# Performance work log

Hardware: AMD Instinct MI355X
Metric: run time of the kernel (lower is better)

Reference implementation:

```python
import jax, jax.numpy as jnp
import numpy as np

B, N, H, NH = 8, 1024, 512, 8
HD = H // NH
SCALE = float(np.sqrt(HD))


def setup_inputs() -> dict:
    key = jax.random.key(0)
    ks = jax.random.split(key, 14)
    s = 0.02
    return {
        "x": jax.random.normal(ks[0], (B, N, H), jnp.float32),
        "distance_matrix": jax.random.uniform(ks[1], (B, N, N), jnp.float32),
        "mask": jax.random.randint(ks[2], (B, N), 0, 2).astype(bool),
        "Wq": jax.random.normal(ks[3], (H, H), jnp.float32) * s,
        "bq": jnp.zeros((H,), jnp.float32),
        "Wk": jax.random.normal(ks[4], (H, H), jnp.float32) * s,
        "bk": jnp.zeros((H,), jnp.float32),
        "Wv": jax.random.normal(ks[5], (H, H), jnp.float32) * s,
        "bv": jnp.zeros((H,), jnp.float32),
        "Wo": jax.random.normal(ks[6], (H, H), jnp.float32) * s,
        "bo": jnp.zeros((H,), jnp.float32),
        "dist_emb": jax.random.normal(ks[7], (50, NH), jnp.float32) * s,
        "attn_bias": jnp.zeros((NH, 1, 1), jnp.float32),
    }


def reference(x, distance_matrix, mask, Wq, bq, Wk, bk, Wv, bv, Wo, bo, dist_emb, attn_bias):
    Bb, Nn, _ = x.shape
    # projections (torch Linear: x @ W.T + b), split heads -> [B, N, NH, HD]
    Q = (x @ Wq.T + bq).reshape(Bb, Nn, NH, HD)
    K = (x @ Wk.T + bk).reshape(Bb, Nn, NH, HD)
    V = (x @ Wv.T + bv).reshape(Bb, Nn, NH, HD)
    # scores [B, NH, N, N]
    scores = jnp.einsum('bqhd,bkhd->bhqk', Q, K) / SCALE
    # distance-bin bias lookup: [B,N,N] -> bins -> [B,N,N,NH] -> [B,NH,N,N]
    bins = jnp.clip((distance_matrix * 10.0).astype(jnp.int32), 0, 49)
    dbias = jnp.transpose(dist_emb[bins], (0, 3, 1, 2))
    scores = scores + dbias + attn_bias[None]  # attn_bias [NH,1,1] broadcasts
    scores = jnp.where(mask[:, None, None, :], -1e9, scores)  # mask over keys
    attn = jax.nn.softmax(scores, axis=-1)  # dropout = identity in eval
    out = jnp.einsum('bhqk,bkhd->bqhd', attn, V).reshape(Bb, Nn, H)
    return out @ Wo.T + bo
```

## Files before the change

kernel.cpp:

```cpp
#include <hip/hip_runtime.h>
#include <hip/hip_bf16.h>
#include <math.h>

#define B_  8
#define N_  1024
#define H_  512
#define NH_ 8
#define HD_ 64

typedef __attribute__((ext_vector_type(8))) short short8;
typedef __attribute__((ext_vector_type(4))) short short4_t;
typedef __attribute__((ext_vector_type(4))) float floatx4;

#define GPTR(p) ((const __attribute__((address_space(1))) void*)(p))
#define LPTR(p) ((__attribute__((address_space(3))) void*)(p))

#define TRB16(dst, addr, IMM) \
    asm volatile("ds_read_b64_tr_b16 %0, %1 offset:" IMM \
                 : "=v"(dst) : "v"(addr) : "memory")

#define EXP2(x) exp2f(x)
#define LOG2E 1.44269504088896f

static __device__ __forceinline__ unsigned short f2bf(float f) {
    __hip_bfloat16 h = __float2bfloat16(f);
    unsigned short u;
    __builtin_memcpy(&u, &h, 2);
    return u;
}

__global__ __launch_bounds__(256) void cvt_all(
    const float* __restrict__ x,  const float* __restrict__ wq,
    const float* __restrict__ wk, const float* __restrict__ wv,
    const float* __restrict__ wo, unsigned short* __restrict__ dst)
{
    const int n4 = (4194304 + 4 * 262144) / 4;
    int i = blockIdx.x * blockDim.x + threadIdx.x;
    const int stride = gridDim.x * blockDim.x;
    for (; i < n4; i += stride) {
        const int e = i * 4;
        const float* src;
        if (e < 4194304) {
            src = x + e;
        } else {
            const int rel = e - 4194304;
            const int w = rel >> 18;
            const int off = rel & 262143;
            src = (w == 0 ? wq : w == 1 ? wk : w == 2 ? wv : wo) + off;
        }
        const float4 v = *(const float4*)src;
        ushort4 r;
        r.x = f2bf(v.x); r.y = f2bf(v.y); r.z = f2bf(v.z); r.w = f2bf(v.w);
        *(ushort4*)(dst + e) = r;
    }
}

__global__ __launch_bounds__(256) void bins_kernel(
    const float* __restrict__ dist, const int* __restrict__ mask,
    unsigned char* __restrict__ bins)
{
    const int gid = blockIdx.x * 256 + threadIdx.x;
    const size_t e = (size_t)gid * 16;
    const int b = gid >> 16;
    const int k = (gid & 63) * 16;
    const float* dsrc = dist + e;
    const int*   msrc = mask + b * N_ + k;

    unsigned w[4];
    #pragma unroll
    for (int i = 0; i < 4; ++i) {
        const float4 v = *(const float4*)(dsrc + 4 * i);
        const int4  mm = *(const int4*)(msrc + 4 * i);
        int b0 = (int)(v.x * 10.f); b0 = b0 < 0 ? 0 : (b0 > 49 ? 49 : b0);
        int b1 = (int)(v.y * 10.f); b1 = b1 < 0 ? 0 : (b1 > 49 ? 49 : b1);
        int b2 = (int)(v.z * 10.f); b2 = b2 < 0 ? 0 : (b2 > 49 ? 49 : b2);
        int b3 = (int)(v.w * 10.f); b3 = b3 < 0 ? 0 : (b3 > 49 ? 49 : b3);
        if (mm.x) b0 = 255;
        if (mm.y) b1 = 255;
        if (mm.z) b2 = 255;
        if (mm.w) b3 = 255;
        w[i] = (unsigned)b0 | ((unsigned)b1 << 8) | ((unsigned)b2 << 16) | ((unsigned)b3 << 24);
    }
    uint4 u; u.x = w[0]; u.y = w[1]; u.z = w[2]; u.w = w[3];
    *(uint4*)(bins + e) = u;
}

template <int BF16OUT>
static __device__ __forceinline__ void gemm_core(
    const unsigned short* __restrict__ A, const unsigned short* __restrict__ W,
    const float* __restrict__ bias, void* __restrict__ C,
    int Ncols, int K, float scale, int row0, int col0)
{
    __shared__ unsigned short As[128 * 32];
    __shared__ unsigned short Bs[128 * 32];

    const int t    = threadIdx.x;
    const int lane = t & 63;
    const int wave = t >> 6;
    const int wr   = wave >> 1;
    const int wc   = wave & 1;
    const int l15  = lane & 15;
    const int lhi  = lane >> 4;

    const int srow = wave * 32 + (lane >> 2);
    const int sk   = (lane & 3) * 8;
    const unsigned short* gA = A + (size_t)(row0 + srow) * K + sk;
    const unsigned short* gB = W + (size_t)(col0 + srow) * K + sk;

    floatx4 acc[4][4];
    #pragma unroll
    for (int m = 0; m < 4; ++m)
        #pragma unroll
        for (int n = 0; n < 4; ++n) acc[m][n] = (floatx4)0.f;

    for (int k0 = 0; k0 < K; k0 += 32) {
        __syncthreads();
        #pragma unroll
        for (int i = 0; i < 2; ++i) {
            __builtin_amdgcn_global_load_lds(GPTR(gA + (size_t)(i * 16) * K + k0),
                                             LPTR(&As[(wave * 32 + i * 16) * 32]), 16, 0, 0);
            __builtin_amdgcn_global_load_lds(GPTR(gB + (size_t)(i * 16) * K + k0),
                                             LPTR(&Bs[(wave * 32 + i * 16) * 32]), 16, 0, 0);
        }
        __syncthreads();

        short8 af[4], bf[4];
        #pragma unroll
        for (int m = 0; m < 4; ++m)
            af[m] = *(const short8*)&As[(wr * 64 + m * 16 + l15) * 32 + lhi * 8];
        #pragma unroll
        for (int n = 0; n < 4; ++n)
            bf[n] = *(const short8*)&Bs[(wc * 64 + n * 16 + l15) * 32 + lhi * 8];
        #pragma unroll
        for (int m = 0; m < 4; ++m)
            #pragma unroll
            for (int n = 0; n < 4; ++n)
                acc[m][n] = __builtin_amdgcn_mfma_f32_16x16x32_bf16(af[m], bf[n], acc[m][n], 0, 0, 0);
    }

    #pragma unroll
    for (int n = 0; n < 4; ++n) {
        const int col = col0 + wc * 64 + n * 16 + l15;
        const float bvv = bias[col];
        #pragma unroll
        for (int m = 0; m < 4; ++m) {
            #pragma unroll
            for (int r = 0; r < 4; ++r) {
                const int row = row0 + wr * 64 + m * 16 + lhi * 4 + r;
                const float v = (acc[m][n][r] + bvv) * scale;
                if (BF16OUT)
                    ((unsigned short*)C)[(size_t)row * Ncols + col] = f2bf(v);
                else
                    ((float*)C)[(size_t)row * Ncols + col] = v;
            }
        }
    }
}

__global__ __launch_bounds__(256) void gemm_qkv(
    const unsigned short* __restrict__ xb,
    const unsigned short* __restrict__ Wq, const unsigned short* __restrict__ Wk,
    const unsigned short* __restrict__ Wv,
    const float* __restrict__ bq, const float* __restrict__ bk,
    const float* __restrict__ bv,
    unsigned short* __restrict__ Qb, unsigned short* __restrict__ Kb,
    unsigned short* __restrict__ Vb)
{
    const int z = blockIdx.z;
    const unsigned short* W = z == 0 ? Wq : (z == 1 ? Wk : Wv);
    const float* bias       = z == 0 ? bq : (z == 1 ? bk : bv);
    unsigned short* C       = z == 0 ? Qb : (z == 1 ? Kb : Vb);
    const float scale       = z == 0 ? (0.125f * LOG2E) : 1.0f;
    gemm_core<1>(xb, W, bias, C, H_, H_, scale, blockIdx.y * 128, blockIdx.x * 128);
}

__global__ __launch_bounds__(256) void gemm_out(
    const unsigned short* __restrict__ Ab, const unsigned short* __restrict__ Wo,
    const float* __restrict__ bo, float* __restrict__ out)
{
    gemm_core<0>(Ab, Wo, bo, out, H_, H_, 1.0f, blockIdx.y * 128, blockIdx.x * 128);
}

__global__ __launch_bounds__(256) void attn_mfma(
    const unsigned short* __restrict__ Qg, const unsigned short* __restrict__ Kg,
    const unsigned short* __restrict__ Vg, const unsigned char* __restrict__ bins,
    const float* __restrict__ demb, const float* __restrict__ abias,
    unsigned short* __restrict__ O)
{
    const int qt = blockIdx.x;
    const int h  = blockIdx.y;
    const int b  = blockIdx.z;
    const int q0 = qt * 64;
    const int t  = threadIdx.x;
    const int lane = t & 63;
    const int wave = t >> 6;
    const int l15 = lane & 15;
    const int lhi = lane >> 4;

    __shared__ unsigned short Ks[64 * 64];
    __shared__ unsigned short Vs[64 * 64];
    __shared__ unsigned short QPs[64 * 64];
    __shared__ unsigned char  Bs[64 * 80];

    float dbl = -1.442695e9f;
    if (lane < 50) dbl = (demb[lane * NH_ + h] + abias[h]) * LOG2E;

    const unsigned short* ksrc[2];
    const unsigned short* vsrc[2];
    #pragma unroll
    for (int i = 0; i < 2; ++i) {
        const int C = wave * 128 + i * 64 + lane;
        const int kr = C >> 3, c = C & 7;
        ksrc[i] = Kg + ((size_t)(b * N_) + kr) * H_ + h * HD_ + ((c ^ (kr & 7)) * 8);
        const int vd16 = C >> 7, rem = C & 127;
        const int krhi = rem >> 3, r2 = rem & 7;
        const int vkr = krhi * 4 + (r2 >> 1), vc = r2 & 1;
        vsrc[i] = Vg + ((size_t)(b * N_) + vkr) * H_ + h * HD_ + vd16 * 16 + vc * 8;
    }
    const unsigned char* bsrc = bins + ((size_t)(b * N_) + q0 + (t >> 2)) * N_ + (t & 3) * 16;
    const int bidx = (t >> 2) * 80 + (t & 3) * 16;

    {
        const int qr = t >> 2;
        const int d0 = (t & 3) * 16;
        const unsigned short* src = Qg + ((size_t)(b * N_ + q0 + qr)) * H_ + h * HD_ + d0;
        #pragma unroll
        for (int cc = 0; cc < 2; ++cc) {
            const uint4 v = *(const uint4*)(src + 8 * cc);
            const int idx = (qr * 64 + d0 + 8 * cc) ^ ((qr & 7) << 3);
            *(uint4*)&QPs[idx] = v;
        }
    }
    __syncthreads();

    short8 aq[2];
    {
        const int qrow = (wave << 4) + l15;
        #pragma unroll
        for (int ck = 0; ck < 2; ++ck) {
            const int kb = lhi * 8 + 32 * ck;
            const int idx = (qrow * 64 + kb) ^ ((qrow & 7) << 3);
            aq[ck] = *(const short8*)&QPs[idx];
        }
    }
    __syncthreads();

    unsigned short* const Pw = &QPs[wave << 10];
    const unsigned trlane = (unsigned)(lhi << 8) + (unsigned)(l15 << 3);
    const unsigned vaddr = (unsigned)(size_t)LPTR(&Vs[0]) + trlane;

    float m = -INFINITY, lsum = 0.f;
    floatx4 o4[4];
    #pragma unroll
    for (int nd = 0; nd < 4; ++nd) o4[nd] = (floatx4)0.f;

    for (int k0 = 0; k0 < N_; k0 += 64) {
        __syncthreads();
        {
            const size_t koff = (size_t)k0;
            #pragma unroll
            for (int i = 0; i < 2; ++i) {
                __builtin_amdgcn_global_load_lds(GPTR(ksrc[i] + koff * H_),
                    LPTR(&Ks[(wave * 128 + i * 64) * 8]), 16, 0, 0);
                __builtin_amdgcn_global_load_lds(GPTR(vsrc[i] + koff * H_),
                    LPTR(&Vs[(wave * 128 + i * 64) * 8]), 16, 0, 0);
            }
            const uint4 brv = *(const uint4*)(bsrc + koff);
            *(uint4*)&Bs[bidx] = brv;
        }
        __syncthreads();

        floatx4 s4[4];
        __builtin_amdgcn_s_setprio(1);
        #pragma unroll
        for (int kn = 0; kn < 4; ++kn) {
            const int kcol = kn * 16 + l15;
            floatx4 acc = (floatx4)0.f;
            #pragma unroll
            for (int ck = 0; ck < 2; ++ck) {
                const int kb = lhi * 8 + 32 * ck;
                const int idx = (kcol * 64 + kb) ^ ((kcol & 7) << 3);
                const short8 bk = *(const short8*)&Ks[idx];
                acc = __builtin_amdgcn_mfma_f32_16x16x32_bf16(bk, aq[ck], acc, 0, 0, 0);
            }
            s4[kn] = acc;
        }
        __builtin_amdgcn_s_setprio(0);

        #pragma unroll
        for (int kn = 0; kn < 4; ++kn) {
            const unsigned bb =
                *(const unsigned*)&Bs[((wave << 4) + l15) * 80 + kn * 16 + (lhi << 2)];
            s4[kn][0] += __shfl(dbl, (int)(bb & 255u), 64);
            s4[kn][1] += __shfl(dbl, (int)((bb >> 8) & 255u), 64);
            s4[kn][2] += __shfl(dbl, (int)((bb >> 16) & 255u), 64);
            s4[kn][3] += __shfl(dbl, (int)(bb >> 24), 64);
        }

        {
            float mx = s4[0][0];
            #pragma unroll
            for (int kn = 0; kn < 4; ++kn)
                #pragma unroll
                for (int r = 0; r < 4; ++r) mx = fmaxf(mx, s4[kn][r]);
            mx = fmaxf(mx, __shfl_xor(mx, 16, 64));
            mx = fmaxf(mx, __shfl_xor(mx, 32, 64));
            const float mnew = fmaxf(m, mx);
            float ts = 0.f;
            #pragma unroll
            for (int kn = 0; kn < 4; ++kn)
                #pragma unroll
                for (int r = 0; r < 4; ++r) {
                    const float p = EXP2(s4[kn][r] - mnew);
                    s4[kn][r] = p;
                    ts += p;
                }
            ts += __shfl_xor(ts, 16, 64);
            ts += __shfl_xor(ts, 32, 64);
            const float alpha = EXP2(m - mnew);
            lsum = lsum * alpha + ts;
            m = mnew;
            #pragma unroll
            for (int r = 0; r < 4; ++r) {
                const float ar = __shfl(alpha, lhi * 4 + r, 64);
                #pragma unroll
                for (int nd = 0; nd < 4; ++nd) o4[nd][r] *= ar;
            }
        }

        #pragma unroll
        for (int kn = 0; kn < 4; ++kn) {
            short4_t pk;
            pk[0] = (short)f2bf(s4[kn][0]);
            pk[1] = (short)f2bf(s4[kn][1]);
            pk[2] = (short)f2bf(s4[kn][2]);
            pk[3] = (short)f2bf(s4[kn][3]);
            const int idx = (l15 * 64 + kn * 16 + (lhi << 2)) ^ ((l15 & 7) << 3);
            *(short4_t*)&Pw[idx] = pk;
        }

        short8 ap[2];
        #pragma unroll
        for (int ck = 0; ck < 2; ++ck) {
            const int idx = (l15 * 64 + ck * 32 + lhi * 8) ^ ((l15 & 7) << 3);
            ap[ck] = *(const short8*)&Pw[idx];
        }
        short4_t v0l[4], v0h[4], v1l[4], v1h[4];
        TRB16(v0l[0], vaddr, "0");    TRB16(v0h[0], vaddr, "128");
        TRB16(v0l[1], vaddr, "2048"); TRB16(v0h[1], vaddr, "2176");
        TRB16(v0l[2], vaddr, "4096"); TRB16(v0h[2], vaddr, "4224");
        TRB16(v0l[3], vaddr, "6144"); TRB16(v0h[3], vaddr, "6272");
        TRB16(v1l[0], vaddr, "1024"); TRB16(v1h[0], vaddr, "1152");
        TRB16(v1l[1], vaddr, "3072"); TRB16(v1h[1], vaddr, "3200");
        TRB16(v1l[2], vaddr, "5120"); TRB16(v1h[2], vaddr, "5248");
        TRB16(v1l[3], vaddr, "7168"); TRB16(v1h[3], vaddr, "7296");
        asm volatile("s_waitcnt lgkmcnt(0)" ::: "memory");
        __builtin_amdgcn_sched_barrier(0);

        __builtin_amdgcn_s_setprio(1);
        #pragma unroll
        for (int nd = 0; nd < 4; ++nd) {
            const short8 bv0 = __builtin_shufflevector(v0l[nd], v0h[nd], 0, 1, 2, 3, 4, 5, 6, 7);
            o4[nd] = __builtin_amdgcn_mfma_f32_16x16x32_bf16(ap[0], bv0, o4[nd], 0, 0, 0);
            const short8 bv1 = __builtin_shufflevector(v1l[nd], v1h[nd], 0, 1, 2, 3, 4, 5, 6, 7);
            o4[nd] = __builtin_amdgcn_mfma_f32_16x16x32_bf16(ap[1], bv1, o4[nd], 0, 0, 0);
        }
        __builtin_amdgcn_s_setprio(0);
    }

    float inv[4];
    #pragma unroll
    for (int r = 0; r < 4; ++r) inv[r] = 1.f / __shfl(lsum, lhi * 4 + r, 64);
    #pragma unroll
    for (int nd = 0; nd < 4; ++nd) {
        const int d = nd * 16 + l15;
        #pragma unroll
        for (int r = 0; r < 4; ++r) {
            const int q = q0 + (wave << 4) + lhi * 4 + r;
            O[((size_t)(b * N_ + q)) * H_ + h * HD_ + d] = f2bf(o4[nd][r] * inv[r]);
        }
    }
}

extern "C" void kernel_launch(void* const* d_in, const int* in_sizes, int n_in,
                              void* d_out, int out_size, void* d_ws, size_t ws_size,
                              hipStream_t stream)
{
    const float* x    = (const float*)d_in[0];
    const float* dist = (const float*)d_in[1];
    const int*   mask = (const int*)d_in[2];
    const float* Wq   = (const float*)d_in[3];
    const float* bq   = (const float*)d_in[4];
    const float* Wk   = (const float*)d_in[5];
    const float* bk   = (const float*)d_in[6];
    const float* Wv   = (const float*)d_in[7];
    const float* bv   = (const float*)d_in[8];
    const float* Wo   = (const float*)d_in[9];
    const float* bo   = (const float*)d_in[10];
    const float* demb = (const float*)d_in[11];
    const float* ab   = (const float*)d_in[12];
    float* out = (float*)d_out;

    const size_t mat = (size_t)B_ * N_ * H_;
    const size_t wsz = (size_t)H_ * H_;

    unsigned short* blob = (unsigned short*)d_ws;
    unsigned short* xb  = blob;
    unsigned short* Wqb = blob + mat;
    unsigned short* Wkb = Wqb + wsz;
    unsigned short* Wvb = Wkb + wsz;
    unsigned short* Wob = Wvb + wsz;
    unsigned short* Qb  = Wob + wsz;
    unsigned short* Kb  = Qb + mat;
    unsigned short* Vb  = Kb + mat;
    unsigned short* Ab  = Vb + mat;
    unsigned char*  binsb = (unsigned char*)(Ab + mat);

    const dim3 blk(256);

    hipLaunchKernelGGL(cvt_all, dim3(1024), blk, 0, stream, x, Wq, Wk, Wv, Wo, blob);
    hipLaunchKernelGGL(bins_kernel, dim3((B_ * N_ * N_) / 16 / 256), blk, 0, stream,
                       dist, mask, binsb);

    const dim3 qgrid(H_ / 128, (B_ * N_) / 128, 3);
    hipLaunchKernelGGL(gemm_qkv, qgrid, blk, 0, stream,
                       xb, Wqb, Wkb, Wvb, bq, bk, bv, Qb, Kb, Vb);

    const dim3 agrid(N_ / 64, NH_, B_);
    hipLaunchKernelGGL(attn_mfma, agrid, blk, 0, stream,
                       Qb, Kb, Vb, binsb, demb, ab, Ab);

    const dim3 ogrid(H_ / 128, (B_ * N_) / 128, 1);
    hipLaunchKernelGGL(gemm_out, ogrid, blk, 0, stream, Ab, Wob, bo, out);
}
```

Measured before the change: 109.5 us.

## Fuse prep kernels, register-prefetch distance bins, skip softmax rescale when max is stable

Merges the bf16 conversion and bin-computation kernels into one launch, partitioned by block index. In the attention kernel, bins are read straight from global memory into registers and prefetched one tile ahead, removing the LDS staging buffer. The online softmax now skips the output rescale when no row max has grown by more than 8 (log2 units) past the running max. This keeps the old max, so probabilities can exceed 1 before normalisation, which adds a small overflow or precision risk.

```diff
diff --git a/kernel.cpp b/kernel.cpp
--- a/kernel.cpp
+++ b/kernel.cpp
@@ -29,60 +29,58 @@
     return u;
 }
 
-__global__ __launch_bounds__(256) void cvt_all(
+__global__ __launch_bounds__(256) void prep_kernel(
     const float* __restrict__ x,  const float* __restrict__ wq,
     const float* __restrict__ wk, const float* __restrict__ wv,
-    const float* __restrict__ wo, unsigned short* __restrict__ dst)
-{
-    const int n4 = (4194304 + 4 * 262144) / 4;
-    int i = blockIdx.x * blockDim.x + threadIdx.x;
-    const int stride = gridDim.x * blockDim.x;
-    for (; i < n4; i += stride) {
-        const int e = i * 4;
-        const float* src;
-        if (e < 4194304) {
-            src = x + e;
-        } else {
-            const int rel = e - 4194304;
-            const int w = rel >> 18;
-            const int off = rel & 262143;
-            src = (w == 0 ? wq : w == 1 ? wk : w == 2 ? wv : wo) + off;
-        }
-        const float4 v = *(const float4*)src;
-        ushort4 r;
-        r.x = f2bf(v.x); r.y = f2bf(v.y); r.z = f2bf(v.z); r.w = f2bf(v.w);
-        *(ushort4*)(dst + e) = r;
-    }
-}
-
-__global__ __launch_bounds__(256) void bins_kernel(
+    const float* __restrict__ wo, unsigned short* __restrict__ dst,
     const float* __restrict__ dist, const int* __restrict__ mask,
     unsigned char* __restrict__ bins)
 {
-    const int gid = blockIdx.x * 256 + threadIdx.x;
-    const size_t e = (size_t)gid * 16;
-    const int b = gid >> 16;
-    const int k = (gid & 63) * 16;
-    const float* dsrc = dist + e;
-    const int*   msrc = mask + b * N_ + k;
-
-    unsigned w[4];
-    #pragma unroll
-    for (int i = 0; i < 4; ++i) {
-        const float4 v = *(const float4*)(dsrc + 4 * i);
-        const int4  mm = *(const int4*)(msrc + 4 * i);
-        int b0 = (int)(v.x * 10.f); b0 = b0 < 0 ? 0 : (b0 > 49 ? 49 : b0);
-        int b1 = (int)(v.y * 10.f); b1 = b1 < 0 ? 0 : (b1 > 49 ? 49 : b1);
-        int b2 = (int)(v.z * 10.f); b2 = b2 < 0 ? 0 : (b2 > 49 ? 49 : b2);
-        int b3 = (int)(v.w * 10.f); b3 = b3 < 0 ? 0 : (b3 > 49 ? 49 : b3);
-        if (mm.x) b0 = 255;
-        if (mm.y) b1 = 255;
-        if (mm.z) b2 = 255;
-        if (mm.w) b3 = 255;
-        w[i] = (unsigned)b0 | ((unsigned)b1 << 8) | ((unsigned)b2 << 16) | ((unsigned)b3 << 24);
-    }
-    uint4 u; u.x = w[0]; u.y = w[1]; u.z = w[2]; u.w = w[3];
-    *(uint4*)(bins + e) = u;
+    const int bid = blockIdx.x;
+    if (bid < 1280) {
+        const int n4 = (4194304 + 4 * 262144) / 4;
+        int i = bid * 256 + threadIdx.x;
+        for (; i < n4; i += 1280 * 256) {
+            const int e = i * 4;
+            const float* src;
+            if (e < 4194304) {
+                src = x + e;
+            } else {
+                const int rel = e - 4194304;
+                const int w = rel >> 18;
+                const int off = rel & 262143;
+                src = (w == 0 ? wq : w == 1 ? wk : w == 2 ? wv : wo) + off;
+            }
+            const float4 v = *(const float4*)src;
+            ushort4 r;
+            r.x = f2bf(v.x); r.y = f2bf(v.y); r.z = f2bf(v.z); r.w = f2bf(v.w);
+            *(ushort4*)(dst + e) = r;
+        }
+    } else {
+        const int gid = (bid - 1280) * 256 + threadIdx.x;
+        const size_t e = (size_t)gid * 16;
+        const int b = gid >> 16;
+        const int k = (gid & 63) * 16;
+        const float* dsrc = dist + e;
+        const int*   msrc = mask + b * N_ + k;
+        unsigned w[4];
+        #pragma unroll
+        for (int i = 0; i < 4; ++i) {
+            const float4 v = *(const float4*)(dsrc + 4 * i);
+            const int4  mm = *(const int4*)(msrc + 4 * i);
+            int b0 = (int)(v.x * 10.f); b0 = b0 < 0 ? 0 : (b0 > 49 ? 49 : b0);
+            int b1 = (int)(v.y * 10.f); b1 = b1 < 0 ? 0 : (b1 > 49 ? 49 : b1);
+            int b2 = (int)(v.z * 10.f); b2 = b2 < 0 ? 0 : (b2 > 49 ? 49 : b2);
+            int b3 = (int)(v.w * 10.f); b3 = b3 < 0 ? 0 : (b3 > 49 ? 49 : b3);
+            if (mm.x) b0 = 255;
+            if (mm.y) b1 = 255;
+            if (mm.z) b2 = 255;
+            if (mm.w) b3 = 255;
+            w[i] = (unsigned)b0 | ((unsigned)b1 << 8) | ((unsigned)b2 << 16) | ((unsigned)b3 << 24);
+        }
+        uint4 u; u.x = w[0]; u.y = w[1]; u.z = w[2]; u.w = w[3];
+        *(uint4*)(bins + e) = u;
+    }
 }
 
 template <int BF16OUT>
@@ -200,7 +198,6 @@
     __shared__ unsigned short Ks[64 * 64];
     __shared__ unsigned short Vs[64 * 64];
     __shared__ unsigned short QPs[64 * 64];
-    __shared__ unsigned char  Bs[64 * 80];
 
     float dbl = -1.442695e9f;
     if (lane < 50) dbl = (demb[lane * NH_ + h] + abias[h]) * LOG2E;
@@ -217,8 +214,8 @@
         const int vkr = krhi * 4 + (r2 >> 1), vc = r2 & 1;
         vsrc[i] = Vg + ((size_t)(b * N_) + vkr) * H_ + h * HD_ + vd16 * 16 + vc * 8;
     }
-    const unsigned char* bsrc = bins + ((size_t)(b * N_) + q0 + (t >> 2)) * N_ + (t & 3) * 16;
-    const int bidx = (t >> 2) * 80 + (t & 3) * 16;
+    const unsigned char* bbase =
+        bins + ((size_t)(b * N_) + q0 + (wave << 4) + l15) * N_ + (lhi << 2);
 
     {
         const int qr = t >> 2;
@@ -231,6 +228,10 @@
             *(uint4*)&QPs[idx] = v;
         }
     }
+    unsigned brC[4], brN[4];
+    #pragma unroll
+    for (int kn = 0; kn < 4; ++kn)
+        brC[kn] = *(const unsigned*)(bbase + kn * 16);
     __syncthreads();
 
     short8 aq[2];
@@ -254,7 +255,8 @@
     #pragma unroll
     for (int nd = 0; nd < 4; ++nd) o4[nd] = (floatx4)0.f;
 
-    for (int k0 = 0; k0 < N_; k0 += 64) {
+    for (int tt = 0; tt < 16; ++tt) {
+        const int k0 = tt * 64;
         __syncthreads();
         {
             const size_t koff = (size_t)k0;
@@ -265,8 +267,11 @@
                 __builtin_amdgcn_global_load_lds(GPTR(vsrc[i] + koff * H_),
                     LPTR(&Vs[(wave * 128 + i * 64) * 8]), 16, 0, 0);
             }
-            const uint4 brv = *(const uint4*)(bsrc + koff);
-            *(uint4*)&Bs[bidx] = brv;
+        }
+        if (tt < 15) {
+            #pragma unroll
+            for (int kn = 0; kn < 4; ++kn)
+                brN[kn] = *(const unsigned*)(bbase + (tt + 1) * 64 + kn * 16);
         }
         __syncthreads();
 
@@ -289,13 +294,14 @@
 
         #pragma unroll
         for (int kn = 0; kn < 4; ++kn) {
-            const unsigned bb =
-                *(const unsigned*)&Bs[((wave << 4) + l15) * 80 + kn * 16 + (lhi << 2)];
+            const unsigned bb = brC[kn];
             s4[kn][0] += __shfl(dbl, (int)(bb & 255u), 64);
             s4[kn][1] += __shfl(dbl, (int)((bb >> 8) & 255u), 64);
             s4[kn][2] += __shfl(dbl, (int)((bb >> 16) & 255u), 64);
             s4[kn][3] += __shfl(dbl, (int)(bb >> 24), 64);
         }
+        #pragma unroll
+        for (int kn = 0; kn < 4; ++kn) brC[kn] = brN[kn];
 
         {
             float mx = s4[0][0];
@@ -305,26 +311,42 @@
                 for (int r = 0; r < 4; ++r) mx = fmaxf(mx, s4[kn][r]);
             mx = fmaxf(mx, __shfl_xor(mx, 16, 64));
             mx = fmaxf(mx, __shfl_xor(mx, 32, 64));
-            const float mnew = fmaxf(m, mx);
-            float ts = 0.f;
-            #pragma unroll
-            for (int kn = 0; kn < 4; ++kn)
+
+            if (__all(mx <= m + 8.f)) {
+                float ts = 0.f;
+                #pragma unroll
+                for (int kn = 0; kn < 4; ++kn)
+                    #pragma unroll
+                    for (int r = 0; r < 4; ++r) {
+                        const float p = EXP2(s4[kn][r] - m);
+                        s4[kn][r] = p;
+                        ts += p;
+                    }
+                ts += __shfl_xor(ts, 16, 64);
+                ts += __shfl_xor(ts, 32, 64);
+                lsum += ts;
+            } else {
+                const float mnew = fmaxf(m, mx);
+                float ts = 0.f;
+                #pragma unroll
+                for (int kn = 0; kn < 4; ++kn)
+                    #pragma unroll
+                    for (int r = 0; r < 4; ++r) {
+                        const float p = EXP2(s4[kn][r] - mnew);
+                        s4[kn][r] = p;
+                        ts += p;
+                    }
+                ts += __shfl_xor(ts, 16, 64);
+                ts += __shfl_xor(ts, 32, 64);
+                const float alpha = EXP2(m - mnew);
+                lsum = lsum * alpha + ts;
+                m = mnew;
                 #pragma unroll
                 for (int r = 0; r < 4; ++r) {
-                    const float p = EXP2(s4[kn][r] - mnew);
-                    s4[kn][r] = p;
-                    ts += p;
+                    const float ar = __shfl(alpha, lhi * 4 + r, 64);
+                    #pragma unroll
+                    for (int nd = 0; nd < 4; ++nd) o4[nd][r] *= ar;
                 }
-            ts += __shfl_xor(ts, 16, 64);
-            ts += __shfl_xor(ts, 32, 64);
-            const float alpha = EXP2(m - mnew);
-            lsum = lsum * alpha + ts;
-            m = mnew;
-            #pragma unroll
-            for (int r = 0; r < 4; ++r) {
-                const float ar = __shfl(alpha, lhi * 4 + r, 64);
-                #pragma unroll
-                for (int nd = 0; nd < 4; ++nd) o4[nd][r] *= ar;
             }
         }
 
@@ -418,9 +440,8 @@
 
     const dim3 blk(256);
 
-    hipLaunchKernelGGL(cvt_all, dim3(1024), blk, 0, stream, x, Wq, Wk, Wv, Wo, blob);
-    hipLaunchKernelGGL(bins_kernel, dim3((B_ * N_ * N_) / 16 / 256), blk, 0, stream,
-                       dist, mask, binsb);
+    hipLaunchKernelGGL(prep_kernel, dim3(3328), blk, 0, stream,
+                       x, Wq, Wk, Wv, Wo, blob, dist, mask, binsb);
 
     const dim3 qgrid(H_ / 128, (B_ * N_) / 128, 3);
     hipLaunchKernelGGL(gemm_qkv, qgrid, blk, 0, stream,
```

After: 140.3 us. 1.28x slower.
